# Performance work log

Hardware: AMD Instinct MI355X
Metric: run time of the kernel (lower is better)

The kernel has to match this reference:

```python
import jax, jax.numpy as jnp
import numpy as np

N_ATOMS = 65536
N_PAIRS = 16777216
N_MOL = 2048
RADIUS = 5.0
ECONV = 14.399645  # eV*Angstrom Coulomb constant


def setup_inputs() -> dict:
    key = jax.random.key(0)
    k1, k2, k3, k4, k5 = jax.random.split(key, 5)
    charges = jax.random.normal(k1, (N_ATOMS, 1), dtype=jnp.float32)
    # distances in (0.5, 1.2*RADIUS): some pairs beyond the screening radius
    pair_dist = jax.random.uniform(k2, (N_PAIRS,), dtype=jnp.float32,
                                   minval=0.5, maxval=1.2 * RADIUS)
    pair_first = jax.random.randint(k3, (N_PAIRS,), 0, N_ATOMS)
    pair_second = jax.random.randint(k4, (N_PAIRS,), 0, N_ATOMS)
    mol_index = jnp.sort(jax.random.randint(k5, (N_ATOMS,), 0, N_MOL))
    return {
        "charges": charges,
        "pair_dist": pair_dist,
        "pair_first": pair_first,
        "pair_second": pair_second,
        "mol_index": mol_index,
        "n_molecules": N_MOL,
    }


def _cosine_screening(pair_dist, radius):
    # smooth cosine screening: 1 at r=0, 0 at r=radius
    return 0.5 * (1.0 + jnp.cos(jnp.pi * pair_dist / radius))


def reference(charges, pair_dist, pair_first, pair_second, mol_index, n_molecules):
    # gather charges for each pair, screened Coulomb per pair  [n_pairs, 1]
    qi = charges[pair_first, 0]
    qj = charges[pair_second, 0]
    base = qi * qj / pair_dist
    scr = _cosine_screening(pair_dist, RADIUS)
    scr = jnp.where(pair_dist < RADIUS, scr, jnp.zeros_like(scr))
    coulomb_pairs = base * scr  # [n_pairs]
    # MolPairSummer: scatter pairs into molecules via mol_index[pair_first]
    pair_mol = mol_index[pair_first]
    coulomb_molecule = jax.ops.segment_sum(coulomb_pairs, pair_mol,
                                           num_segments=n_molecules)
    coulomb_molecule = 0.5 * ECONV * coulomb_molecule
    return coulomb_molecule[:, None]  # [n_molecules, 1]
```

## Files before the change

kernel.cpp:

```cpp
#include <hip/hip_runtime.h>
#include <hip/hip_fp16.h>


constexpr float RADIUS = 5.0f;
constexpr float ECONV  = 14.399645f;

typedef float f4 __attribute__((ext_vector_type(4)));
typedef int   i4 __attribute__((ext_vector_type(4)));

__global__ __launch_bounds__(256) void prep_mol(const int* __restrict__ mol,
                                                uint2* __restrict__ rec, int nchunk) {
    int c = blockIdx.x * 256 + threadIdx.x;
    if (c >= nchunk) return;
    const int* p = mol + c * 32;
    int base = p[0];
    unsigned mask = 0;
    int prev = base;
#pragma unroll
    for (int i = 1; i < 32; ++i) {
        int m = p[i];
        if (m != prev) mask |= (1u << i);
        prev = m;
    }
    rec[c] = make_uint2(mask, (unsigned)base);
}

__global__ __launch_bounds__(1024) void pair_bins(const f4* __restrict__ dist4,
                                                  const i4* __restrict__ first4,
                                                  const i4* __restrict__ second4,
                                                  const float* __restrict__ qf32,
                                                  const uint2* __restrict__ molrec_g,
                                                  float* __restrict__ partial,
                                                  int nvec, int n_atoms, int n_mol) {
    extern __shared__ char smem[];
    float* bins = (float*)smem;
    uint2* mrec = (uint2*)(smem + (size_t)n_mol * 4);
    const int nchunk = n_atoms >> 5;
    __half* qt = (__half*)(smem + (size_t)n_mol * 4 + (size_t)nchunk * 8);

    for (int m = threadIdx.x; m < n_mol; m += 1024) bins[m] = 0.0f;
    for (int c = threadIdx.x; c < nchunk; c += 1024) mrec[c] = molrec_g[c];
    {
        const f4* src = (const f4*)qf32;
        int nv = n_atoms >> 2;
        for (int i = threadIdx.x; i < nv; i += 1024) {
            f4 q = src[i];
            __half2* dst = (__half2*)(qt + (size_t)i * 4);
            dst[0] = __floats2half2_rn(q.x, q.y);
            dst[1] = __floats2half2_rn(q.z, q.w);
        }
    }
    __syncthreads();

    const float c_rad = 3.14159265358979323846f / RADIUS;
    const int stride = gridDim.x * 1024;
    const int v0 = blockIdx.x * 1024 + threadIdx.x;

    int vc = v0;
    bool pc_ = vc < nvec; int ac = pc_ ? vc : 0;
    f4 dc = __builtin_nontemporal_load(dist4 + ac);
    i4 fc = __builtin_nontemporal_load(first4 + ac);
    i4 sc = __builtin_nontemporal_load(second4 + ac);
    int vn = v0 + stride;
    bool pn_ = vn < nvec; int an = pn_ ? vn : 0;
    f4 dn = __builtin_nontemporal_load(dist4 + an);
    i4 fn = __builtin_nontemporal_load(first4 + an);
    i4 sn = __builtin_nontemporal_load(second4 + an);

    for (int vt = v0 + 2 * stride; pc_; vt += stride) {
        bool pt_ = vt < nvec; int at = pt_ ? vt : 0;
        f4 dt = __builtin_nontemporal_load(dist4 + at);
        i4 ft = __builtin_nontemporal_load(first4 + at);
        i4 st = __builtin_nontemporal_load(second4 + at);

#pragma unroll
        for (int k = 0; k < 4; ++k) {
            const int f = fc[k];
            const int s = sc[k];
            const uint2 r = mrec[f >> 5];
            const int mi = (int)r.y + __popc(r.x & ((2u << (f & 31)) - 1u));
            const float qi = __half2float(qt[f]);
            const float qj = __half2float(qt[s]);
            const float d  = dc[k];
            const float scr = (d < RADIUS) ? 0.5f * (1.0f + __cosf(d * c_rad)) : 0.0f;
            const float val = qi * qj * __fdividef(scr, d);
            atomicAdd(&bins[mi], val);
        }

        dc = dn; fc = fn; sc = sn; pc_ = pn_;
        dn = dt; fn = ft; sn = st; pn_ = pt_;
    }

    __syncthreads();
    float* p = partial + (size_t)blockIdx.x * n_mol;
    for (int m = threadIdx.x; m < n_mol; m += 1024) p[m] = bins[m];
}

__global__ __launch_bounds__(256) void reduce_full(const float* __restrict__ partial,
                                                   float* __restrict__ out,
                                                   int nblk, int n_mol) {
    int m = blockIdx.x * 256 + threadIdx.x;
    if (m >= n_mol) return;
    float s0 = 0.f, s1 = 0.f, s2 = 0.f, s3 = 0.f;
    int b = 0;
    for (; b + 4 <= nblk; b += 4) {
        s0 += partial[(size_t)(b + 0) * n_mol + m];
        s1 += partial[(size_t)(b + 1) * n_mol + m];
        s2 += partial[(size_t)(b + 2) * n_mol + m];
        s3 += partial[(size_t)(b + 3) * n_mol + m];
    }
    for (; b < nblk; ++b) s0 += partial[(size_t)b * n_mol + m];
    out[m] = 0.5f * ECONV * ((s0 + s1) + (s2 + s3));
}

extern "C" void kernel_launch(void* const* d_in, const int* in_sizes, int n_in,
                              void* d_out, int out_size, void* d_ws, size_t ws_size,
                              hipStream_t stream) {
    const float* charges     = (const float*)d_in[0];
    const float* pair_dist   = (const float*)d_in[1];
    const int*   pair_first  = (const int*)d_in[2];
    const int*   pair_second = (const int*)d_in[3];
    const int*   mol_index   = (const int*)d_in[4];
    const int n_atoms = in_sizes[0];
    const int n_pairs = in_sizes[1];
    const int n_mol   = out_size;
    const int nvec    = n_pairs >> 2;
    const int nchunk  = n_atoms >> 5;

    uint2* molrec = (uint2*)d_ws;
    size_t off = ((size_t)nchunk * 8 + 255) & ~(size_t)255;
    float* partial = (float*)((char*)d_ws + off);

    const int nblk = 256;
    const size_t smem_bytes = (size_t)n_mol * 4 + (size_t)nchunk * 8 + (size_t)n_atoms * 2;
    hipFuncSetAttribute((const void*)pair_bins,
                        hipFuncAttributeMaxDynamicSharedMemorySize,
                        (int)smem_bytes);

    prep_mol<<<(nchunk + 255) / 256, 256, 0, stream>>>(mol_index, molrec, nchunk);
    pair_bins<<<nblk, 1024, smem_bytes, stream>>>((const f4*)pair_dist,
                                                  (const i4*)pair_first,
                                                  (const i4*)pair_second,
                                                  charges, molrec, partial,
                                                  nvec, n_atoms, n_mol);
    reduce_full<<<(n_mol + 255) / 256, 256, 0, stream>>>(partial, (float*)d_out, nblk, n_mol);
}
```

Measured before the change: 281.3 us.

## Stage pair indices into LDS via async global_load_lds double buffering

```diff
diff --git a/kernel.cpp b/kernel.cpp
--- a/kernel.cpp
+++ b/kernel.cpp
@@ -4,9 +4,18 @@
 
 constexpr float RADIUS = 5.0f;
 constexpr float ECONV  = 14.399645f;
+#define NMOL_BYTES   8192
+#define TILE         1024
+#define TILE_BYTES   8192
+#define QT_OFF       24576
 
 typedef float f4 __attribute__((ext_vector_type(4)));
-typedef int   i4 __attribute__((ext_vector_type(4)));
+
+#define AS1 __attribute__((address_space(1)))
+#define AS3 __attribute__((address_space(3)))
+__device__ __forceinline__ void gld_lds16(const void* g, void* l) {
+    __builtin_amdgcn_global_load_lds((const AS1 void*)g, (AS3 void*)l, 16, 0, 0);
+}
 
 __global__ __launch_bounds__(256) void prep_mol(const int* __restrict__ mol,
                                                 uint2* __restrict__ rec, int nchunk) {
@@ -25,75 +34,80 @@
     rec[c] = make_uint2(mask, (unsigned)base);
 }
 
-__global__ __launch_bounds__(1024) void pair_bins(const f4* __restrict__ dist4,
-                                                  const i4* __restrict__ first4,
-                                                  const i4* __restrict__ second4,
-                                                  const float* __restrict__ qf32,
-                                                  const uint2* __restrict__ molrec_g,
-                                                  float* __restrict__ partial,
-                                                  int nvec, int n_atoms, int n_mol) {
+__global__ __launch_bounds__(1024) void pair_bins(
+    const float* __restrict__ dist,
+    const unsigned* __restrict__ first,
+    const unsigned* __restrict__ second,
+    const float* __restrict__ qf32,
+    const uint2* __restrict__ mrec,
+    float* __restrict__ partial,
+    int pairs_per_block, int n_atoms, int n_mol)
+{
     extern __shared__ char smem[];
-    float* bins = (float*)smem;
-    uint2* mrec = (uint2*)(smem + (size_t)n_mol * 4);
-    const int nchunk = n_atoms >> 5;
-    __half* qt = (__half*)(smem + (size_t)n_mol * 4 + (size_t)nchunk * 8);
+    float*  bins  = (float*)smem;
+    char*   tiles = smem + NMOL_BYTES;
+    __half* qt    = (__half*)(smem + QT_OFF);
 
-    for (int m = threadIdx.x; m < n_mol; m += 1024) bins[m] = 0.0f;
-    for (int c = threadIdx.x; c < nchunk; c += 1024) mrec[c] = molrec_g[c];
+    const int tid  = threadIdx.x;
+    const int w    = tid >> 6;
+    const int lane = tid & 63;
+    const int base = blockIdx.x * pairs_per_block;
+    const int nt   = pairs_per_block / TILE;
+
+    for (int m = tid; m < n_mol; m += 1024) bins[m] = 0.0f;
     {
         const f4* src = (const f4*)qf32;
         int nv = n_atoms >> 2;
-        for (int i = threadIdx.x; i < nv; i += 1024) {
+        for (int i = tid; i < nv; i += 1024) {
             f4 q = src[i];
             __half2* dst = (__half2*)(qt + (size_t)i * 4);
             dst[0] = __floats2half2_rn(q.x, q.y);
             dst[1] = __floats2half2_rn(q.z, q.w);
         }
     }
+    if (w < 8) {
+        const unsigned* src = ((w < 4) ? first : second) + base + ((w & 3) << 8);
+        char* dst = tiles + ((w >= 4) ? 4096 : 0) + ((w & 3) << 10);
+        gld_lds16(src + (lane << 2), dst);
+    }
+    float d_cur = dist[base + tid];
     __syncthreads();
 
     const float c_rad = 3.14159265358979323846f / RADIUS;
-    const int stride = gridDim.x * 1024;
-    const int v0 = blockIdx.x * 1024 + threadIdx.x;
+    int cur = 0;
 
-    int vc = v0;
-    bool pc_ = vc < nvec; int ac = pc_ ? vc : 0;
-    f4 dc = __builtin_nontemporal_load(dist4 + ac);
-    i4 fc = __builtin_nontemporal_load(first4 + ac);
-    i4 sc = __builtin_nontemporal_load(second4 + ac);
-    int vn = v0 + stride;
-    bool pn_ = vn < nvec; int an = pn_ ? vn : 0;
-    f4 dn = __builtin_nontemporal_load(dist4 + an);
-    i4 fn = __builtin_nontemporal_load(first4 + an);
-    i4 sn = __builtin_nontemporal_load(second4 + an);
-
-    for (int vt = v0 + 2 * stride; pc_; vt += stride) {
-        bool pt_ = vt < nvec; int at = pt_ ? vt : 0;
-        f4 dt = __builtin_nontemporal_load(dist4 + at);
-        i4 ft = __builtin_nontemporal_load(first4 + at);
-        i4 st = __builtin_nontemporal_load(second4 + at);
-
-#pragma unroll
-        for (int k = 0; k < 4; ++k) {
-            const int f = fc[k];
-            const int s = sc[k];
-            const uint2 r = mrec[f >> 5];
-            const int mi = (int)r.y + __popc(r.x & ((2u << (f & 31)) - 1u));
-            const float qi = __half2float(qt[f]);
-            const float qj = __half2float(qt[s]);
-            const float d  = dc[k];
-            const float scr = (d < RADIUS) ? 0.5f * (1.0f + __cosf(d * c_rad)) : 0.0f;
-            const float val = qi * qj * __fdividef(scr, d);
-            atomicAdd(&bins[mi], val);
+    for (int t = 0; t < nt; ++t) {
+        float d_nxt = 0.0f;
+        if (t + 1 < nt) {
+            const int nb = base + (t + 1) * TILE;
+            if (w < 8) {
+                const unsigned* src = ((w < 4) ? first : second) + nb + ((w & 3) << 8);
+                char* dst = tiles + (cur ^ 1) * TILE_BYTES
+                          + ((w >= 4) ? 4096 : 0) + ((w & 3) << 10);
+                gld_lds16(src + (lane << 2), dst);
+            }
+            d_nxt = dist[nb + tid];
         }
 
-        dc = dn; fc = fn; sc = sn; pc_ = pn_;
-        dn = dt; fn = ft; sn = st; pn_ = pt_;
+        const int* ftile = (const int*)(tiles + cur * TILE_BYTES);
+        const int* stile = (const int*)(tiles + cur * TILE_BYTES + 4096);
+        const int f = ftile[tid];
+        const int s = stile[tid];
+        const uint2 r = mrec[f >> 5];
+        const int mi = (int)r.y + __popc(r.x & ((2u << (f & 31)) - 1u));
+        const float qi = __half2float(qt[f]);
+        const float qj = __half2float(qt[s]);
+        const float d  = d_cur;
+        const float scr = (d < RADIUS) ? 0.5f * (1.0f + __cosf(d * c_rad)) : 0.0f;
+        atomicAdd(&bins[mi], qi * qj * __fdividef(scr, d));
+
+        __syncthreads();
+        d_cur = d_nxt;
+        cur ^= 1;
     }
 
-    __syncthreads();
     float* p = partial + (size_t)blockIdx.x * n_mol;
-    for (int m = threadIdx.x; m < n_mol; m += 1024) p[m] = bins[m];
+    for (int m = tid; m < n_mol; m += 1024) p[m] = bins[m];
 }
 
 __global__ __launch_bounds__(256) void reduce_full(const float* __restrict__ partial,
@@ -118,30 +132,29 @@
                               hipStream_t stream) {
     const float* charges     = (const float*)d_in[0];
     const float* pair_dist   = (const float*)d_in[1];
-    const int*   pair_first  = (const int*)d_in[2];
-    const int*   pair_second = (const int*)d_in[3];
+    const unsigned* pair_first  = (const unsigned*)d_in[2];
+    const unsigned* pair_second = (const unsigned*)d_in[3];
     const int*   mol_index   = (const int*)d_in[4];
     const int n_atoms = in_sizes[0];
     const int n_pairs = in_sizes[1];
     const int n_mol   = out_size;
-    const int nvec    = n_pairs >> 2;
     const int nchunk  = n_atoms >> 5;
+
+    const int nblk = 256;
+    const int ppb  = n_pairs / nblk;
 
     uint2* molrec = (uint2*)d_ws;
     size_t off = ((size_t)nchunk * 8 + 255) & ~(size_t)255;
     float* partial = (float*)((char*)d_ws + off);
 
-    const int nblk = 256;
-    const size_t smem_bytes = (size_t)n_mol * 4 + (size_t)nchunk * 8 + (size_t)n_atoms * 2;
+    const size_t smem_bytes = (size_t)QT_OFF + (size_t)n_atoms * 2;
     hipFuncSetAttribute((const void*)pair_bins,
                         hipFuncAttributeMaxDynamicSharedMemorySize,
                         (int)smem_bytes);
 
     prep_mol<<<(nchunk + 255) / 256, 256, 0, stream>>>(mol_index, molrec, nchunk);
-    pair_bins<<<nblk, 1024, smem_bytes, stream>>>((const f4*)pair_dist,
-                                                  (const i4*)pair_first,
-                                                  (const i4*)pair_second,
+    pair_bins<<<nblk, 1024, smem_bytes, stream>>>(pair_dist, pair_first, pair_second,
                                                   charges, molrec, partial,
-                                                  nvec, n_atoms, n_mol);
+                                                  ppb, n_atoms, n_mol);
     reduce_full<<<(n_mol + 255) / 256, 256, 0, stream>>>(partial, (float*)d_out, nblk, n_mol);
 }
```

Result: slower. 314.9 us (+12.0%).

## Use inline-asm quad-buffered contiguous block loads with explicit vmcnt waits

Applied to the files above, without the earlier changes.

```diff
diff --git a/kernel.cpp b/kernel.cpp
--- a/kernel.cpp
+++ b/kernel.cpp
@@ -25,25 +25,58 @@
     rec[c] = make_uint2(mask, (unsigned)base);
 }
 
-__global__ __launch_bounds__(1024) void pair_bins(const f4* __restrict__ dist4,
-                                                  const i4* __restrict__ first4,
-                                                  const i4* __restrict__ second4,
-                                                  const float* __restrict__ qf32,
-                                                  const uint2* __restrict__ molrec_g,
-                                                  float* __restrict__ partial,
-                                                  int nvec, int n_atoms, int n_mol) {
+#define LOAD3(D, F, S, VOFF)                                                   \
+    asm volatile("global_load_dwordx4 %0, %3, %4\n\t"                          \
+                 "global_load_dwordx4 %1, %3, %5\n\t"                          \
+                 "global_load_dwordx4 %2, %3, %6"                              \
+                 : "=&v"(D), "=&v"(F), "=&v"(S)                                \
+                 : "v"(VOFF), "s"(dist), "s"(first), "s"(second)               \
+                 : "memory")
+
+#define WAITV(N)                                                               \
+    asm volatile("s_waitcnt vmcnt(" #N ")" ::: "memory");                      \
+    __builtin_amdgcn_sched_barrier(0)
+
+#define PROC(DD, FF, SS)                                                       \
+    do {                                                                       \
+        _Pragma("unroll")                                                      \
+        for (int k = 0; k < 4; ++k) {                                          \
+            const int f = (FF)[k];                                             \
+            const int s = (SS)[k];                                             \
+            const uint2 r = mrec[f >> 5];                                      \
+            const int mi = (int)r.y + __popc(r.x & ((2u << (f & 31)) - 1u));   \
+            const float qi = __half2float(qt[f]);                              \
+            const float qj = __half2float(qt[s]);                              \
+            const float d = (DD)[k];                                           \
+            const float scr = (d < RADIUS) ? 0.5f * (1.0f + __cosf(d * c_rad)) \
+                                           : 0.0f;                             \
+            atomicAdd(&bins[mi], qi * qj * __fdividef(scr, d));                \
+        }                                                                      \
+    } while (0)
+
+__global__ __launch_bounds__(1024, 4) void pair_bins(
+    const float* __restrict__ dist,
+    const int* __restrict__ first,
+    const int* __restrict__ second,
+    const float* __restrict__ qf32,
+    const uint2* __restrict__ molrec_g,
+    float* __restrict__ partial,
+    int pairs_per_block, int n_atoms, int n_mol)
+{
     extern __shared__ char smem[];
     float* bins = (float*)smem;
     uint2* mrec = (uint2*)(smem + (size_t)n_mol * 4);
     const int nchunk = n_atoms >> 5;
     __half* qt = (__half*)(smem + (size_t)n_mol * 4 + (size_t)nchunk * 8);
 
-    for (int m = threadIdx.x; m < n_mol; m += 1024) bins[m] = 0.0f;
-    for (int c = threadIdx.x; c < nchunk; c += 1024) mrec[c] = molrec_g[c];
+    const int tid = threadIdx.x;
+
+    for (int m = tid; m < n_mol; m += 1024) bins[m] = 0.0f;
+    for (int c = tid; c < nchunk; c += 1024) mrec[c] = molrec_g[c];
     {
         const f4* src = (const f4*)qf32;
         int nv = n_atoms >> 2;
-        for (int i = threadIdx.x; i < nv; i += 1024) {
+        for (int i = tid; i < nv; i += 1024) {
             f4 q = src[i];
             __half2* dst = (__half2*)(qt + (size_t)i * 4);
             dst[0] = __floats2half2_rn(q.x, q.y);
@@ -53,47 +86,37 @@
     __syncthreads();
 
     const float c_rad = 3.14159265358979323846f / RADIUS;
-    const int stride = gridDim.x * 1024;
-    const int v0 = blockIdx.x * 1024 + threadIdx.x;
 
-    int vc = v0;
-    bool pc_ = vc < nvec; int ac = pc_ ? vc : 0;
-    f4 dc = __builtin_nontemporal_load(dist4 + ac);
-    i4 fc = __builtin_nontemporal_load(first4 + ac);
-    i4 sc = __builtin_nontemporal_load(second4 + ac);
-    int vn = v0 + stride;
-    bool pn_ = vn < nvec; int an = pn_ ? vn : 0;
-    f4 dn = __builtin_nontemporal_load(dist4 + an);
-    i4 fn = __builtin_nontemporal_load(first4 + an);
-    i4 sn = __builtin_nontemporal_load(second4 + an);
+    const int nvec_blk = pairs_per_block >> 2;
+    const int NB = nvec_blk >> 12;
+    unsigned voffA = (unsigned)(blockIdx.x * nvec_blk + tid) * 16u;
+    unsigned voffB = voffA + 16384u;
+    unsigned voffC = voffA + 32768u;
+    unsigned voffD = voffA + 49152u;
+    const unsigned BSTRIDE = 65536u;
 
-    for (int vt = v0 + 2 * stride; pc_; vt += stride) {
-        bool pt_ = vt < nvec; int at = pt_ ? vt : 0;
-        f4 dt = __builtin_nontemporal_load(dist4 + at);
-        i4 ft = __builtin_nontemporal_load(first4 + at);
-        i4 st = __builtin_nontemporal_load(second4 + at);
+    f4 dA, dB, dC, dD;
+    i4 fA, fB, fC, fD, sA, sB, sC, sD;
 
-#pragma unroll
-        for (int k = 0; k < 4; ++k) {
-            const int f = fc[k];
-            const int s = sc[k];
-            const uint2 r = mrec[f >> 5];
-            const int mi = (int)r.y + __popc(r.x & ((2u << (f & 31)) - 1u));
-            const float qi = __half2float(qt[f]);
-            const float qj = __half2float(qt[s]);
-            const float d  = dc[k];
-            const float scr = (d < RADIUS) ? 0.5f * (1.0f + __cosf(d * c_rad)) : 0.0f;
-            const float val = qi * qj * __fdividef(scr, d);
-            atomicAdd(&bins[mi], val);
-        }
+    LOAD3(dA, fA, sA, voffA);
+    LOAD3(dB, fB, sB, voffB);
+    LOAD3(dC, fC, sC, voffC);
+    LOAD3(dD, fD, sD, voffD);
 
-        dc = dn; fc = fn; sc = sn; pc_ = pn_;
-        dn = dt; fn = ft; sn = st; pn_ = pt_;
+    for (int t = 0; t < NB - 1; ++t) {
+        WAITV(9); PROC(dA, fA, sA); voffA += BSTRIDE; LOAD3(dA, fA, sA, voffA);
+        WAITV(9); PROC(dB, fB, sB); voffB += BSTRIDE; LOAD3(dB, fB, sB, voffB);
+        WAITV(9); PROC(dC, fC, sC); voffC += BSTRIDE; LOAD3(dC, fC, sC, voffC);
+        WAITV(9); PROC(dD, fD, sD); voffD += BSTRIDE; LOAD3(dD, fD, sD, voffD);
     }
+    WAITV(9); PROC(dA, fA, sA);
+    WAITV(6); PROC(dB, fB, sB);
+    WAITV(3); PROC(dC, fC, sC);
+    WAITV(0); PROC(dD, fD, sD);
 
     __syncthreads();
     float* p = partial + (size_t)blockIdx.x * n_mol;
-    for (int m = threadIdx.x; m < n_mol; m += 1024) p[m] = bins[m];
+    for (int m = tid; m < n_mol; m += 1024) p[m] = bins[m];
 }
 
 __global__ __launch_bounds__(256) void reduce_full(const float* __restrict__ partial,
@@ -124,24 +147,23 @@
     const int n_atoms = in_sizes[0];
     const int n_pairs = in_sizes[1];
     const int n_mol   = out_size;
-    const int nvec    = n_pairs >> 2;
     const int nchunk  = n_atoms >> 5;
+
+    const int nblk = 256;
+    const int ppb  = n_pairs / nblk;
 
     uint2* molrec = (uint2*)d_ws;
     size_t off = ((size_t)nchunk * 8 + 255) & ~(size_t)255;
     float* partial = (float*)((char*)d_ws + off);
 
-    const int nblk = 256;
     const size_t smem_bytes = (size_t)n_mol * 4 + (size_t)nchunk * 8 + (size_t)n_atoms * 2;
     hipFuncSetAttribute((const void*)pair_bins,
                         hipFuncAttributeMaxDynamicSharedMemorySize,
                         (int)smem_bytes);
 
     prep_mol<<<(nchunk + 255) / 256, 256, 0, stream>>>(mol_index, molrec, nchunk);
-    pair_bins<<<nblk, 1024, smem_bytes, stream>>>((const f4*)pair_dist,
-                                                  (const i4*)pair_first,
-                                                  (const i4*)pair_second,
+    pair_bins<<<nblk, 1024, smem_bytes, stream>>>(pair_dist, pair_first, pair_second,
                                                   charges, molrec, partial,
-                                                  nvec, n_atoms, n_mol);
+                                                  ppb, n_atoms, n_mol);
     reduce_full<<<(n_mol + 255) / 256, 256, 0, stream>>>(partial, (float*)d_out, nblk, n_mol);
 }
```

Result: faster. 266.9 us (-5.1%).
